# Kernel tuning notes

Measured on AMD Instinct MI355X. Metric: run time of the kernel, lower is better.

## Reference

```python
import jax, jax.numpy as jnp
import numpy as np

EMBED = 64
NHEADS = 8
DK = EMBED // NHEADS          # 8
PS = 32                       # patchsize[log2(8)] = (32, 32) for every head


def lrelu(z):
    return jnp.where(z > 0, z, 0.2 * z)


def conv1x1(x, w, b):
    # x: [B,C,H,W], w: [O,C], b: [O]
    return jnp.einsum('oc,bchw->bohw', w, x) + b[None, :, None, None]


def conv3x3_reflect(x, w, b, dilation=1):
    p = dilation  # pad == dilation keeps spatial size for k=3
    xp = jnp.pad(x, ((0, 0), (0, 0), (p, p), (p, p)), mode='reflect')
    y = jax.lax.conv_general_dilated(
        xp, w, window_strides=(1, 1), padding='VALID',
        rhs_dilation=(dilation, dilation),
        dimension_numbers=('NCHW', 'OIHW', 'NCHW'))
    return y + b[None, :, None, None]


def setup_inputs() -> dict:
    key = jax.random.key(0)
    ks = jax.random.split(key, 16)
    B, C, H, W = 8, EMBED, 256, 256
    g = 0.02
    inp = {
        'x': jax.random.normal(ks[0], (B, C, H, W), jnp.float32),
        'm': jax.random.uniform(ks[1], (B, 1, H, W), jnp.float32),
        'wq': jax.random.normal(ks[2], (C, C), jnp.float32) * g,
        'bq': jnp.zeros((C,), jnp.float32),
        'wk': jax.random.normal(ks[3], (C, C), jnp.float32) * g,
        'bk': jnp.zeros((C,), jnp.float32),
        'wv': jax.random.normal(ks[4], (C, C), jnp.float32) * g,
        'bv': jnp.zeros((C,), jnp.float32),
        'wo': jax.random.normal(ks[5], (C, C, 3, 3), jnp.float32) * g,
        'bo': jnp.zeros((C,), jnp.float32),
        'wf1': jax.random.normal(ks[6], (C, C, 3, 3), jnp.float32) * g,
        'bf1': jnp.zeros((C,), jnp.float32),
        'wf2': jax.random.normal(ks[7], (C, C, 3, 3), jnp.float32) * g,
        'bf2': jnp.zeros((C,), jnp.float32),
    }
    return inp


def _window(t, b, oh, ow):
    # [B, C, H, W] -> [B, nH, oh*ow, dk*ps*ps] (head = channel chunk)
    t = t.reshape(b, NHEADS, DK, oh, PS, ow, PS)
    t = t.transpose(0, 1, 3, 5, 2, 4, 6)
    return t.reshape(b, NHEADS, oh * ow, DK * PS * PS)


def _forward(x, m, wq, bq, wk, bk, wv, bv, wo, bo, wf1, bf1, wf2, bf2):
    b, c, h, w = x.shape
    oh, ow = h // PS, w // PS
    q = _window(conv1x1(x, wq, bq), b, oh, ow)
    k = _window(conv1x1(x, wk, bk), b, oh, ow)
    v = _window(conv1x1(x, wv, bv), b, oh, ow)
    # NOTE: original code calls scores.masked_fill(mm, -1e9) non-in-place and
    # discards the result, so the mask `m` does NOT affect the math. Faithful.
    scale = 1.0 / jnp.sqrt(jnp.asarray(DK * PS * PS, x.dtype))
    scores = jnp.einsum('bhqe,bhke->bhqk', q, k) * scale  # [B,nH,oh*ow,oh*ow]
    p = jax.nn.softmax(scores, axis=-1)
    y = jnp.einsum('bhqk,bhke->bhqe', p, v)
    # un-window back to [B, C, H, W] (head order == channel-chunk order)
    y = y.reshape(b, NHEADS, oh, ow, DK, PS, PS)
    y = y.transpose(0, 1, 4, 2, 5, 3, 6).reshape(b, c, h, w)
    x1 = x + lrelu(conv3x3_reflect(y, wo, bo))
    ff = lrelu(conv3x3_reflect(x1, wf1, bf1, dilation=2))
    ff = lrelu(conv3x3_reflect(ff, wf2, bf2, dilation=1))
    return x1 + ff


def reference(x, m, wq, bq, wk, bk, wv, bv, wo, bo, wf1, bf1, wf2, bf2):
    return _forward(x, m, wq, bq, wk, bk, wv, bv, wo, bo, wf1, bf1, wf2, bf2)
```

## Files before the change

kernel.cpp:

```cpp
#include <hip/hip_runtime.h>
#include <hip/hip_fp16.h>

#define SCALE 0.011048543456039806f

typedef _Float16 half8 __attribute__((ext_vector_type(8)));
typedef _Float16 h4    __attribute__((ext_vector_type(4)));
typedef float f32x4 __attribute__((ext_vector_type(4)));
typedef unsigned int uint32;

__global__ __launch_bounds__(256) void prep_kernel(const float* __restrict__ wq,
                                                   const float* __restrict__ wk,
                                                   const float* __restrict__ wv,
                                                   const float* __restrict__ wo,
                                                   const float* __restrict__ wf1,
                                                   const float* __restrict__ wf2,
                                                   float* __restrict__ scr) {
    int i = blockIdx.x * 256 + threadIdx.x;
    if (i < 262144) { scr[i] = 0.f; return; }
    __half* wh = (__half*)(scr + 262144);
    int j = i - 262144;
    if (j < 12288) {
        int gm = j >> 6, c = j & 63;
        int mtx = gm >> 6, o = gm & 63;
        const float* src = (mtx == 0) ? wq : ((mtx == 1) ? wk : wv);
        wh[j] = __float2half(src[o * 64 + c]);
    } else {
        int r = j - 12288;
        int mtx = r / 36864;
        int q2 = r - mtx * 36864;
        int tap = q2 >> 12;
        int oc = q2 & 4095;
        int o = oc >> 6, c = oc & 63;
        const float* src = (mtx == 0) ? wo : ((mtx == 1) ? wf1 : wf2);
        wh[j] = __float2half(src[(o * 64 + c) * 9 + tap]);
    }
}

__global__ __launch_bounds__(512) void qkv_mfma(const float* __restrict__ x,
                                                const __half* __restrict__ wqkv,
                                                const float* __restrict__ bq,
                                                const float* __restrict__ bk,
                                                const float* __restrict__ bv,
                                                __half* __restrict__ q,
                                                __half* __restrict__ k,
                                                __half* __restrict__ v) {
    __shared__ __align__(16) __half Xs[256 * 72];
    __shared__ __align__(16) __half Ws[192 * 72];
    int t = threadIdx.x;
    int bx = blockIdx.x;
    int b = bx >> 8, row = bx & 255;
    int hw0 = row << 8;
    int bbase = b << 22;

    for (int i = 0; i < 32; i++) {
        int idx = i * 512 + t;
        int c = idx >> 8, p = idx & 255;
        Xs[p * 72 + c] = __float2half(x[bbase + (c << 16) + hw0 + p]);
    }
    const uint32* src = (const uint32*)wqkv;
    #pragma unroll
    for (int i = 0; i < 12; i++) {
        int idx = i * 512 + t;
        int o = idx >> 5, c2 = idx & 31;
        *(uint32*)&Ws[o * 72 + c2 * 2] = src[idx];
    }
    __syncthreads();

    int wave = t >> 6, lane = t & 63;
    int l15 = lane & 15, quad = lane >> 4;
    int mg = wave >> 2, ng = wave & 3;
    f32x4 acc[4][6];
    #pragma unroll
    for (int i = 0; i < 4; i++)
        #pragma unroll
        for (int m = 0; m < 6; m++) acc[i][m] = (f32x4){0.f, 0.f, 0.f, 0.f};

    #pragma unroll
    for (int kc = 0; kc < 2; kc++) {
        half8 af[6];
        #pragma unroll
        for (int m = 0; m < 6; m++)
            af[m] = *(const half8*)&Ws[((mg * 6 + m) * 16 + l15) * 72 + kc * 32 + quad * 8];
        #pragma unroll
        for (int i = 0; i < 4; i++) {
            half8 bf = *(const half8*)&Xs[(ng * 64 + i * 16 + l15) * 72 + kc * 32 + quad * 8];
            #pragma unroll
            for (int m = 0; m < 6; m++)
                acc[i][m] = __builtin_amdgcn_mfma_f32_16x16x32_f16(af[m], bf, acc[i][m], 0, 0, 0);
        }
    }
    #pragma unroll
    for (int i = 0; i < 4; i++) {
        int pix = hw0 + ng * 64 + i * 16 + l15;
        #pragma unroll
        for (int m = 0; m < 6; m++) {
            int gm = mg * 6 + m;
            int mtx = gm >> 2;
            int ob = (gm & 3) * 16 + quad * 4;
            __half* dst = (mtx == 0) ? q : ((mtx == 1) ? k : v);
            const float* bb = (mtx == 0) ? bq : ((mtx == 1) ? bk : bv);
            #pragma unroll
            for (int r = 0; r < 4; r++) {
                float z = acc[i][m][r] + bb[ob + r];
                dst[bbase + ((ob + r) << 16) + pix] = __float2half(z);
            }
        }
    }
}

__global__ __launch_bounds__(256) void scores_kernel(const __half* __restrict__ q,
                                                     const __half* __restrict__ k,
                                                     float* __restrict__ sc) {
    __shared__ float Qs[64][68];
    __shared__ float Ks[64][68];
    int ec = blockIdx.x;
    int bh = blockIdx.y;
    int b = bh >> 3, h = bh & 7;
    int cbase = ((b * 64 + h * 8 + ec) << 16);
    int t = threadIdx.x;
    int qg = t >> 4, kg = t & 15;
    float acc[4][4] = {};
    for (int j = 0; j < 16; j++) {
        __syncthreads();
        #pragma unroll
        for (int i = 0; i < 16; i++) {
            int idx = i * 256 + t;
            int wi = idx >> 6;
            int el = idx & 63;
            int eg = j * 64 + el;
            int py = eg >> 5, px = eg & 31;
            int oy = wi >> 3, ox = wi & 7;
            int a = cbase + ((oy * 32 + py) << 8) + ox * 32 + px;
            Qs[el][wi] = __half2float(q[a]);
            Ks[el][wi] = __half2float(k[a]);
        }
        __syncthreads();
        for (int e = 0; e < 64; e++) {
            float4 qv = *(const float4*)&Qs[e][qg * 4];
            float4 kv = *(const float4*)&Ks[e][kg * 4];
            float qa[4] = {qv.x, qv.y, qv.z, qv.w};
            float ka[4] = {kv.x, kv.y, kv.z, kv.w};
            #pragma unroll
            for (int i = 0; i < 4; i++)
                #pragma unroll
                for (int jj = 0; jj < 4; jj++)
                    acc[i][jj] += qa[i] * ka[jj];
        }
    }
    float* dst = sc + bh * 4096;
    #pragma unroll
    for (int i = 0; i < 4; i++)
        #pragma unroll
        for (int jj = 0; jj < 4; jj++)
            atomicAdd(&dst[(qg * 4 + i) * 64 + kg * 4 + jj], acc[i][jj]);
}

__global__ __launch_bounds__(64) void softmax_kernel(float* __restrict__ sc) {
    int row = blockIdx.x;
    int ki = threadIdx.x;
    float s = sc[row * 64 + ki] * SCALE;
    float m = s;
    #pragma unroll
    for (int off = 32; off; off >>= 1) m = fmaxf(m, __shfl_xor(m, off));
    float e = __expf(s - m);
    float sum = e;
    #pragma unroll
    for (int off = 32; off; off >>= 1) sum += __shfl_xor(sum, off);
    sc[row * 64 + ki] = e / sum;
}

__global__ __launch_bounds__(256) void attnout_kernel(const float* __restrict__ p,
                                                      const __half* __restrict__ v,
                                                      __half* __restrict__ y) {
    __shared__ float Ps[64][65];
    __shared__ float Vs[64][132];
    int dk = blockIdx.x, bh = blockIdx.y;
    int b = bh >> 3, h = bh & 7;
    int cbase = ((b * 64 + h * 8 + dk) << 16);
    int t = threadIdx.x;
    #pragma unroll
    for (int i = 0; i < 16; i++) {
        int idx = i * 256 + t;
        Ps[idx >> 6][idx & 63] = p[bh * 4096 + idx];
    }
    int qg = t >> 4, eg = t & 15;
    for (int sub = 0; sub < 8; sub++) {
        __syncthreads();
        #pragma unroll
        for (int i = 0; i < 32; i++) {
            int idx = i * 256 + t;
            int ki = idx >> 7, el = idx & 127;
            int elg = sub * 128 + el;
            int py = elg >> 5, px = elg & 31;
            int oy = ki >> 3, ox = ki & 7;
            Vs[ki][el] = __half2float(v[cbase + ((oy * 32 + py) << 8) + ox * 32 + px]);
        }
        __syncthreads();
        float acc[4][8] = {};
        for (int ki = 0; ki < 64; ki++) {
            float4 v0 = *(const float4*)&Vs[ki][eg * 8];
            float4 v1 = *(const float4*)&Vs[ki][eg * 8 + 4];
            #pragma unroll
            for (int i = 0; i < 4; i++) {
                float pv = Ps[qg * 4 + i][ki];
                acc[i][0] += pv * v0.x; acc[i][1] += pv * v0.y;
                acc[i][2] += pv * v0.z; acc[i][3] += pv * v0.w;
                acc[i][4] += pv * v1.x; acc[i][5] += pv * v1.y;
                acc[i][6] += pv * v1.z; acc[i][7] += pv * v1.w;
            }
        }
        int elg0 = sub * 128 + eg * 8;
        int py = elg0 >> 5, px = elg0 & 31;
        #pragma unroll
        for (int i = 0; i < 4; i++) {
            int wi = qg * 4 + i;
            int oy = wi >> 3, ox = wi & 7;
            int a = cbase + ((oy * 32 + py) << 8) + ox * 32 + px;
            #pragma unroll
            for (int jj = 0; jj < 8; jj++)
                y[a + jj] = __float2half(acc[i][jj]);
        }
    }
}

template <int DIL, int IN_NCHW, int RES, int OUTM>
__global__ __launch_bounds__(256) void conv3x3_v2(const _Float16* __restrict__ in,
                                                  const _Float16* __restrict__ wt,
                                                  const float* __restrict__ bias,
                                                  const void* __restrict__ res,
                                                  void* __restrict__ out) {
    constexpr int TH = 8, TW = 32;
    constexpr int PH = TH + 2 * DIL, PW = TW + 2 * DIL;
    constexpr int NP = PH * PW;
    __shared__ __align__(16) _Float16 Xs[NP * 64];

    int t = threadIdx.x;
    int wave = t >> 6, lane = t & 63;
    int bx = blockIdx.x;
    int tc = bx & 7, tr = (bx >> 3) & 31, b = bx >> 8;
    int x0 = tc * TW, y0 = tr * TH;
    int bb = b << 22;

    if (IN_NCHW) {
        constexpr int PO = (NP + 7) / 8;
        constexpr int SIT = (PO * 8 * 64) / 256;
        for (int i = 0; i < SIT; i++) {
            int s = i * 256 + t;
            int l = s & 63, G = s >> 6;
            int p = (G >> 3) * 8 + (l & 7);
            int c = (G & 7) * 8 + (l >> 3);
            int py = p / PW, px = p - py * PW;
            int gy = y0 + py - DIL; gy = gy < 0 ? -gy : (gy > 255 ? 510 - gy : gy);
            int gx = x0 + px - DIL; gx = gx < 0 ? -gx : (gx > 255 ? 510 - gx : gx);
            _Float16 val = in[bb + (c << 16) + (gy << 8) + gx];
            if (p < NP)
                Xs[(p << 6) + (((c >> 3) ^ (p & 7)) << 3) + (c & 7)] = val;
        }
    } else {
        constexpr int SLOTS = NP * 8;
        constexpr int SIT = (SLOTS + 255) / 256;
        half8 tmp[SIT];
        #pragma unroll
        for (int i = 0; i < SIT; i++) {
            int s = i * 256 + t;
            int p = s >> 3, c8 = s & 7;
            int py = p / PW, px = p - py * PW;
            int gy = y0 + py - DIL; gy = gy < 0 ? -gy : (gy > 255 ? 510 - gy : gy);
            int gx = x0 + px - DIL; gx = gx < 0 ? -gx : (gx > 255 ? 510 - gx : gx);
            tmp[i] = *(const half8*)(in + bb + (((gy << 8) + gx) << 6) + c8 * 8);
        }
        #pragma unroll
        for (int i = 0; i < SIT; i++) {
            int s = i * 256 + t;
            int p = s >> 3, c8 = s & 7;
            if (s < SLOTS)
                *(half8*)&Xs[(p << 6) + ((c8 ^ (p & 7)) << 3)] = tmp[i];
        }
    }

    int l15 = lane & 15, quad = lane >> 4;
    half8 af[9][2];
    #pragma unroll
    for (int tap = 0; tap < 9; tap++)
        #pragma unroll
        for (int kc = 0; kc < 2; kc++)
            af[tap][kc] = *(const half8*)&wt[tap * 4096 + (wave * 16 + l15) * 64 + kc * 32 + quad * 8];

    f32x4 acc[16];
    #pragma unroll
    for (int nt = 0; nt < 16; nt++) acc[nt] = (f32x4){0.f, 0.f, 0.f, 0.f};

    __syncthreads();

    #pragma unroll
    for (int tap = 0; tap < 9; tap++) {
        const int ky = tap / 3, kx = tap % 3;
        #pragma unroll
        for (int kc = 0; kc < 2; kc++) {
            int cq = kc * 4 + quad;
            #pragma unroll
            for (int nt = 0; nt < 16; nt++) {
                int p = ((nt >> 1) + ky * DIL) * PW + (nt & 1) * 16 + kx * DIL + l15;
                half8 bf = *(const half8*)&Xs[(p << 6) + ((cq ^ (p & 7)) << 3)];
                acc[nt] = __builtin_amdgcn_mfma_f32_16x16x32_f16(af[tap][kc], bf, acc[nt], 0, 0, 0);
            }
        }
    }

    int oc0 = wave * 16 + quad * 4;
    f32x4 b4 = *(const f32x4*)&bias[oc0];
    #pragma unroll
    for (int nt = 0; nt < 16; nt++) {
        int pixg = ((y0 + (nt >> 1)) << 8) + x0 + (nt & 1) * 16 + l15;
        float z[4];
        #pragma unroll
        for (int r = 0; r < 4; r++) {
            float w = acc[nt][r] + b4[r];
            z[r] = w > 0.f ? w : 0.2f * w;
        }
        if (RES == 1) {
            const float* rf = (const float*)res;
            #pragma unroll
            for (int r = 0; r < 4; r++) z[r] += rf[bb + ((oc0 + r) << 16) + pixg];
        } else if (RES == 2) {
            h4 rv = *(const h4*)((const _Float16*)res + bb + (pixg << 6) + oc0);
            #pragma unroll
            for (int r = 0; r < 4; r++) z[r] += (float)rv[r];
        }
        if (OUTM == 0) {
            h4 ov;
            #pragma unroll
            for (int r = 0; r < 4; r++) ov[r] = (_Float16)z[r];
            *(h4*)((_Float16*)out + bb + (pixg << 6) + oc0) = ov;
        } else {
            #pragma unroll
            for (int r = 0; r < 4; r++)
                ((float*)out)[bb + ((oc0 + r) << 16) + pixg] = z[r];
        }
    }
}

extern "C" void kernel_launch(void* const* d_in, const int* in_sizes, int n_in,
                              void* d_out, int out_size, void* d_ws, size_t ws_size,
                              hipStream_t stream) {
    const float* x   = (const float*)d_in[0];
    float*       scr = (float*)d_in[1];
    const float* wq  = (const float*)d_in[2];
    const float* bq  = (const float*)d_in[3];
    const float* wk  = (const float*)d_in[4];
    const float* bk  = (const float*)d_in[5];
    const float* wv  = (const float*)d_in[6];
    const float* bv  = (const float*)d_in[7];
    const float* wo  = (const float*)d_in[8];
    const float* bo  = (const float*)d_in[9];
    const float* wf1 = (const float*)d_in[10];
    const float* bf1 = (const float*)d_in[11];
    const float* wf2 = (const float*)d_in[12];
    const float* bf2 = (const float*)d_in[13];

    __half* wsA  = (__half*)d_ws;
    __half* wsB  = (__half*)((char*)d_ws + 67108864);
    __half* vbuf = (__half*)d_out;
    __half* ybuf = vbuf + 33554432;
    float*  outf = (float*)d_out;
    float*  sc   = scr;
    const __half* wh    = (const __half*)(scr + 262144);
    const __half* wqkv  = wh;
    const _Float16* wTo = (const _Float16*)(wh + 12288);
    const _Float16* wT1 = (const _Float16*)(wh + 12288 + 36864);
    const _Float16* wT2 = (const _Float16*)(wh + 12288 + 73728);

    prep_kernel<<<1504, 256, 0, stream>>>(wq, wk, wv, wo, wf1, wf2, scr);
    qkv_mfma<<<2048, 512, 0, stream>>>(x, wqkv, bq, bk, bv, wsA, wsB, vbuf);
    scores_kernel<<<dim3(8, 64), 256, 0, stream>>>(wsA, wsB, sc);
    softmax_kernel<<<4096, 64, 0, stream>>>(sc);
    attnout_kernel<<<dim3(8, 64), 256, 0, stream>>>(sc, vbuf, ybuf);
    conv3x3_v2<1, 1, 1, 0><<<2048, 256, 0, stream>>>((const _Float16*)ybuf, wTo, bo,
                                                     (const void*)x, (void*)wsA);
    conv3x3_v2<2, 0, 0, 0><<<2048, 256, 0, stream>>>((const _Float16*)wsA, wT1, bf1,
                                                     nullptr, (void*)wsB);
    conv3x3_v2<1, 0, 2, 1><<<2048, 256, 0, stream>>>((const _Float16*)wsB, wT2, bf2,
                                                     (const void*)wsA, (void*)outf);
}
```

Measured before the change: 964.9 us.

## Cut conv3x3 register pressure and use square tiles for dilated conv

The conv3x3 kernel no longer preloads all 18 weight fragments into registers. It now loads the two fragments for each tap inside the tap loop, and the launch bound requests 3 blocks per CU to raise occupancy. The dilation-2 conv switches from an 8x32 tile to a 16x16 tile, which shrinks the halo in shared memory and the redundant loads. In exchange, weight loads now sit inside the MFMA loop and may add latency there.

After: 1.931 ms. 2x slower.

```diff
diff --git a/kernel.cpp b/kernel.cpp
--- a/kernel.cpp
+++ b/kernel.cpp
@@ -224,20 +224,23 @@
 }
 
 template <int DIL, int IN_NCHW, int RES, int OUTM>
-__global__ __launch_bounds__(256) void conv3x3_v2(const _Float16* __restrict__ in,
-                                                  const _Float16* __restrict__ wt,
-                                                  const float* __restrict__ bias,
-                                                  const void* __restrict__ res,
-                                                  void* __restrict__ out) {
-    constexpr int TH = 8, TW = 32;
+__global__ __launch_bounds__(256, 3) void conv3x3_v3(const _Float16* __restrict__ in,
+                                                     const _Float16* __restrict__ wt,
+                                                     const float* __restrict__ bias,
+                                                     const void* __restrict__ res,
+                                                     void* __restrict__ out) {
+    constexpr int TH = (DIL == 2) ? 16 : 8;
+    constexpr int TW = (DIL == 2) ? 16 : 32;
+    constexpr int NB = TW / 16;
     constexpr int PH = TH + 2 * DIL, PW = TW + 2 * DIL;
     constexpr int NP = PH * PW;
+    constexpr int NTC = 256 / TW;
     __shared__ __align__(16) _Float16 Xs[NP * 64];
 
     int t = threadIdx.x;
     int wave = t >> 6, lane = t & 63;
     int bx = blockIdx.x;
-    int tc = bx & 7, tr = (bx >> 3) & 31, b = bx >> 8;
+    int tc = bx % NTC, tr = (bx / NTC) % (256 / TH), b = bx >> 8;
     int x0 = tc * TW, y0 = tr * TH;
     int bb = b << 22;
 
@@ -279,12 +282,7 @@
     }
 
     int l15 = lane & 15, quad = lane >> 4;
-    half8 af[9][2];
-    #pragma unroll
-    for (int tap = 0; tap < 9; tap++)
-        #pragma unroll
-        for (int kc = 0; kc < 2; kc++)
-            af[tap][kc] = *(const half8*)&wt[tap * 4096 + (wave * 16 + l15) * 64 + kc * 32 + quad * 8];
+    const _Float16* wrow = wt + (wave * 16 + l15) * 64 + quad * 8;
 
     f32x4 acc[16];
     #pragma unroll
@@ -295,14 +293,17 @@
     #pragma unroll
     for (int tap = 0; tap < 9; tap++) {
         const int ky = tap / 3, kx = tap % 3;
+        half8 afA = *(const half8*)&wrow[tap * 4096];
+        half8 afB = *(const half8*)&wrow[tap * 4096 + 32];
         #pragma unroll
         for (int kc = 0; kc < 2; kc++) {
+            half8 af = kc ? afB : afA;
             int cq = kc * 4 + quad;
             #pragma unroll
             for (int nt = 0; nt < 16; nt++) {
-                int p = ((nt >> 1) + ky * DIL) * PW + (nt & 1) * 16 + kx * DIL + l15;
+                int p = (nt / NB + ky * DIL) * PW + (nt % NB) * 16 + kx * DIL + l15;
                 half8 bf = *(const half8*)&Xs[(p << 6) + ((cq ^ (p & 7)) << 3)];
-                acc[nt] = __builtin_amdgcn_mfma_f32_16x16x32_f16(af[tap][kc], bf, acc[nt], 0, 0, 0);
+                acc[nt] = __builtin_amdgcn_mfma_f32_16x16x32_f16(af, bf, acc[nt], 0, 0, 0);
             }
         }
     }
@@ -311,7 +312,7 @@
     f32x4 b4 = *(const f32x4*)&bias[oc0];
     #pragma unroll
     for (int nt = 0; nt < 16; nt++) {
-        int pixg = ((y0 + (nt >> 1)) << 8) + x0 + (nt & 1) * 16 + l15;
+        int pixg = ((y0 + nt / NB) << 8) + x0 + (nt % NB) * 16 + l15;
         float z[4];
         #pragma unroll
         for (int r = 0; r < 4; r++) {
@@ -375,10 +376,10 @@
     scores_kernel<<<dim3(8, 64), 256, 0, stream>>>(wsA, wsB, sc);
     softmax_kernel<<<4096, 64, 0, stream>>>(sc);
     attnout_kernel<<<dim3(8, 64), 256, 0, stream>>>(sc, vbuf, ybuf);
-    conv3x3_v2<1, 1, 1, 0><<<2048, 256, 0, stream>>>((const _Float16*)ybuf, wTo, bo,
+    conv3x3_v3<1, 1, 1, 0><<<2048, 256, 0, stream>>>((const _Float16*)ybuf, wTo, bo,
                                                      (const void*)x, (void*)wsA);
-    conv3x3_v2<2, 0, 0, 0><<<2048, 256, 0, stream>>>((const _Float16*)wsA, wT1, bf1,
+    conv3x3_v3<2, 0, 0, 0><<<2048, 256, 0, stream>>>((const _Float16*)wsA, wT1, bf1,
                                                      nullptr, (void*)wsB);
-    conv3x3_v2<1, 0, 2, 1><<<2048, 256, 0, stream>>>((const _Float16*)wsB, wT2, bf2,
+    conv3x3_v3<1, 0, 2, 1><<<2048, 256, 0, stream>>>((const _Float16*)wsB, wT2, bf2,
                                                      (const void*)wsA, (void*)outf);
 }
```
